# Kernel optimization log

Hardware: AMD Instinct MI355X
Metric: run time of the kernel (lower is better)

## Reference

```python
import jax, jax.numpy as jnp
import numpy as np

# (in_dim, hidden1, out_dim) for each torchvision MLP block
_DIMS = {"i": (3, 20, 100), "c": (10, 8, 1), "s": (17, 34, 17), "m": (100, 20, 100),
         "n": (100, 20, 100), "t": (200, 20, 100), "k": (300, 100, 100), "p": (100, 30, 3)}

def setup_inputs():
    key = jax.random.key(0)
    keys = iter(jax.random.split(key, 64))
    inp = {"x": jax.random.normal(next(keys), (14, 17, 10, 3), jnp.float32)}
    for p, (din, h1, h2) in _DIMS.items():
        inp[p + "W1"] = jax.random.normal(next(keys), (din, h1), jnp.float32) * 0.1
        inp[p + "b1"] = jnp.zeros((h1,), jnp.float32)
        inp[p + "g"] = jnp.ones((h1,), jnp.float32)
        inp[p + "B"] = jnp.zeros((h1,), jnp.float32)
        inp[p + "W2"] = jax.random.normal(next(keys), (h1, h2), jnp.float32) * 0.1
        inp[p + "b2"] = jnp.zeros((h2,), jnp.float32)
    return inp

def _ln(h, g, B):
    mu = jnp.mean(h, -1, keepdims=True)
    var = jnp.mean((h - mu) ** 2, -1, keepdims=True)
    return (h - mu) / jnp.sqrt(var + 1e-5) * g + B

def _mlp(x, W1, b1, g, B, W2, b2):
    # torchvision.ops.MLP([h1, h2]): Linear -> LayerNorm -> ReLU -> (dropout=id in eval) -> Linear
    h = jax.nn.relu(_ln(x @ W1 + b1, g, B))
    return h @ W2 + b2

def reference(x, iW1, ib1, ig, iB, iW2, ib2, cW1, cb1, cg, cB, cW2, cb2,
              sW1, sb1, sg, sB, sW2, sb2, mW1, mb1, mg, mB, mW2, mb2,
              nW1, nb1, ng, nB, nW2, nb2, tW1, tb1, tg, tB, tW2, tb2,
              kW1, kb1, kg, kB, kW2, kb2, pW1, pb1, pg, pB, pW2, pb2):
    h = _mlp(x, iW1, ib1, ig, iB, iW2, ib2)              # [14,17,10,100]
    h = jnp.swapaxes(h, -1, -2)                          # [14,17,100,10]
    h = _mlp(h, cW1, cb1, cg, cB, cW2, cb2)[..., 0]      # [14,17,100]
    h = jnp.swapaxes(h, -1, -2)                          # [14,100,17]
    h = _mlp(h, sW1, sb1, sg, sB, sW2, sb2)              # [14,100,17]
    h = jnp.swapaxes(h, -1, -2)                          # [14,17,100]
    # vectorized over the 10 center frames i = 2..11 (replaces the Python loop)
    mf = _mlp(h[1:11] - h[0:10], mW1, mb1, mg, mB, mW2, mb2)                      # [10,17,100]
    pf = _mlp(h[1:11], nW1, nb1, ng, nB, nW2, nb2)
    pf = _mlp(jnp.concatenate([pf, mf], -1), tW1, tb1, tg, tB, tW2, tb2)          # [10,17,100]
    mb_ = _mlp(h[4:14] - h[3:13], mW1, mb1, mg, mB, mW2, mb2)
    nf = _mlp(h[3:13], nW1, nb1, ng, nB, nW2, nb2)
    nf = _mlp(jnp.concatenate([nf, mb_], -1), tW1, tb1, tg, tB, tW2, tb2)         # [10,17,100]
    comb = _mlp(jnp.concatenate([pf, h[2:12], nf], -1), kW1, kb1, kg, kB, kW2, kb2)  # [10,17,100]
    # original writes out[0..9] of a zeros(12,17,100) buffer; rows 10,11 stay zero
    out = jnp.concatenate([comb, jnp.zeros((2, 17, 100), comb.dtype)], 0)         # [12,17,100]
    return _mlp(out, pW1, pb1, pg, pB, pW2, pb2)         # [12,17,3]
```

## Files before the change

### kernel.cpp

```cpp
#include <hip/hip_runtime.h>

#define T 512
#define NS1 70
#define ZBLK 240
#define FLAG_BYTE 98304
#define MAGIC 0x51A6E1D0C0FFEEULL

__device__ __forceinline__ float wave_sum_all(float v){
    #pragma unroll
    for (int off = 1; off < 64; off <<= 1) v += __shfl_xor(v, off, 64);
    return v;
}

__device__ __forceinline__ void cpa(const float* __restrict__ src, float* dst, int n, int t){
    int g4 = n >> 2;
    for (int g = t; g < g4; g += T) {
        __builtin_amdgcn_global_load_lds(
            (const __attribute__((address_space(1))) void*)(src + g*4),
            (__attribute__((address_space(3))) void*)(dst + g*4), 16, 0, 0);
    }
    for (int i = (g4<<2) + t; i < n; i += T) dst[i] = src[i];
}

struct S1 {
    alignas(16) float u[170][20];
    alignas(16) float h2s[17][20];
    alignas(16) float spre[20][34];
    alignas(16) float iW2[2000];
    alignas(16) float ib2[100];
    alignas(16) float cW1[80];
    alignas(16) float cb1[8];
    alignas(16) float cg[8];
    alignas(16) float cB[8];
    alignas(16) float cW2[8];
    alignas(16) float cb2s[4];
    alignas(16) float sW1[578];
    alignas(16) float sb1[36];
    alignas(16) float sg[36];
    alignas(16) float sB[36];
    alignas(16) float sW2[578];
    alignas(16) float sb2[20];
};
struct S2 {
    alignas(16) float inrow[4][100];
    alignas(16) float hid4[4][20];
    alignas(16) float v4[4][100];
    alignas(16) float hidT[2][20];
    alignas(16) float kin[300];
    alignas(16) float kpart[5][100];
    alignas(16) float khid[100];
    alignas(16) float comb[100];
    alignas(16) float ppart[4][32];
    alignas(16) float mW1[2000]; alignas(16) float mb1[20]; alignas(16) float mg[20];
    alignas(16) float mB[20];    alignas(16) float mW2[2000]; alignas(16) float mb2[100];
    alignas(16) float nW1[2000]; alignas(16) float nb1[20]; alignas(16) float ng[20];
    alignas(16) float nB[20];    alignas(16) float nW2[2000]; alignas(16) float nb2[100];
    alignas(16) float tW1[4000]; alignas(16) float tb1[20]; alignas(16) float tg[20];
    alignas(16) float tB[20];    alignas(16) float tW2[2000]; alignas(16) float tb2[100];
    alignas(16) float kb1[100];  alignas(16) float kg[100];  alignas(16) float kB[100];
    alignas(16) float kW2[10000]; alignas(16) float kb2[100];
    alignas(16) float pW1[3000]; alignas(16) float pb1[32]; alignas(16) float pg[32];
    alignas(16) float pB[32];    alignas(16) float pW2[92]; alignas(16) float pb2[4];
};
union SMem { S1 s1; S2 s2; };

__global__ __launch_bounds__(T) void k_fused(
    const float* __restrict__ x,
    const float* __restrict__ iW1, const float* __restrict__ ib1,
    const float* __restrict__ ig,  const float* __restrict__ iB,
    const float* __restrict__ iW2, const float* __restrict__ ib2,
    const float* __restrict__ cW1, const float* __restrict__ cb1,
    const float* __restrict__ cg,  const float* __restrict__ cB,
    const float* __restrict__ cW2, const float* __restrict__ cb2,
    const float* __restrict__ sW1, const float* __restrict__ sb1,
    const float* __restrict__ sg,  const float* __restrict__ sB,
    const float* __restrict__ sW2, const float* __restrict__ sb2,
    const float* __restrict__ mW1, const float* __restrict__ mb1,
    const float* __restrict__ mg,  const float* __restrict__ mB,
    const float* __restrict__ mW2, const float* __restrict__ mb2,
    const float* __restrict__ nW1, const float* __restrict__ nb1,
    const float* __restrict__ ng,  const float* __restrict__ nB,
    const float* __restrict__ nW2, const float* __restrict__ nb2,
    const float* __restrict__ tW1, const float* __restrict__ tb1,
    const float* __restrict__ tg,  const float* __restrict__ tB,
    const float* __restrict__ tW2, const float* __restrict__ tb2,
    const float* __restrict__ kW1, const float* __restrict__ kb1,
    const float* __restrict__ kg,  const float* __restrict__ kB,
    const float* __restrict__ kW2, const float* __restrict__ kb2,
    const float* __restrict__ pW1, const float* __restrict__ pb1,
    const float* __restrict__ pg,  const float* __restrict__ pB,
    const float* __restrict__ pW2, const float* __restrict__ pb2,
    float* __restrict__ h_ws, unsigned long long* __restrict__ flagS,
    float* __restrict__ out)
{
    const int bid = blockIdx.x;
    const int t = threadIdx.x;
    const int lane = t & 63, wv = t >> 6;
    __shared__ SMem sm;

    if (bid < NS1) {
        S1& s = sm.s1;
        cpa(iW2, s.iW2, 2000, t); cpa(ib2, s.ib2, 100, t);
        cpa(cW1, s.cW1, 80, t);   cpa(cb1, s.cb1, 8, t);  cpa(cg, s.cg, 8, t);
        cpa(cB, s.cB, 8, t);      cpa(cW2, s.cW2, 8, t);  cpa(cb2, s.cb2s, 1, t);
        cpa(sW1, s.sW1, 578, t);  cpa(sb1, s.sb1, 34, t); cpa(sg, s.sg, 34, t);
        cpa(sB, s.sB, 34, t);     cpa(sW2, s.sW2, 578, t); cpa(sb2, s.sb2, 17, t);

        const int a = bid / 5, d0 = (bid % 5) * 20;

        if (t < 170) {
            const float* xr = x + (a*170 + t)*3;
            float x0 = xr[0], x1 = xr[1], x2 = xr[2];
            float pre[20];
            float mu = 0.f;
            #pragma unroll
            for (int j = 0; j < 20; ++j) {
                float v = ib1[j] + x0*iW1[j] + x1*iW1[20+j] + x2*iW1[40+j];
                pre[j] = v; mu += v;
            }
            mu *= 0.05f;
            float var = 0.f;
            #pragma unroll
            for (int j = 0; j < 20; ++j) { float d = pre[j]-mu; var = fmaf(d,d,var); }
            float inv = rsqrtf(var*0.05f + 1e-5f);
            #pragma unroll
            for (int j = 0; j < 20; ++j) {
                float v = (pre[j]-mu)*inv*ig[j] + iB[j];
                s.u[t][j] = v > 0.f ? v : 0.f;
            }
        }
        __syncthreads();

        if (t < 340) {
            int b = t / 20, dd = t % 20, d = d0 + dd;
            float w[8];
            #pragma unroll
            for (int j = 0; j < 8; ++j) w[j] = s.cb1[j];
            float bias = s.ib2[d];
            #pragma unroll 2
            for (int c = 0; c < 10; ++c) {
                const float4* ur = (const float4*)s.u[b*10 + c];
                float4 u0=ur[0], u1=ur[1], u2=ur[2], u3=ur[3], u4=ur[4];
                float acc = bias;
                acc=fmaf(u0.x,s.iW2[0*100+d],acc);  acc=fmaf(u0.y,s.iW2[1*100+d],acc);
                acc=fmaf(u0.z,s.iW2[2*100+d],acc);  acc=fmaf(u0.w,s.iW2[3*100+d],acc);
                acc=fmaf(u1.x,s.iW2[4*100+d],acc);  acc=fmaf(u1.y,s.iW2[5*100+d],acc);
                acc=fmaf(u1.z,s.iW2[6*100+d],acc);  acc=fmaf(u1.w,s.iW2[7*100+d],acc);
                acc=fmaf(u2.x,s.iW2[8*100+d],acc);  acc=fmaf(u2.y,s.iW2[9*100+d],acc);
                acc=fmaf(u2.z,s.iW2[10*100+d],acc); acc=fmaf(u2.w,s.iW2[11*100+d],acc);
                acc=fmaf(u3.x,s.iW2[12*100+d],acc); acc=fmaf(u3.y,s.iW2[13*100+d],acc);
                acc=fmaf(u3.z,s.iW2[14*100+d],acc); acc=fmaf(u3.w,s.iW2[15*100+d],acc);
                acc=fmaf(u4.x,s.iW2[16*100+d],acc); acc=fmaf(u4.y,s.iW2[17*100+d],acc);
                acc=fmaf(u4.z,s.iW2[18*100+d],acc); acc=fmaf(u4.w,s.iW2[19*100+d],acc);
                #pragma unroll
                for (int j = 0; j < 8; ++j) w[j] = fmaf(acc, s.cW1[c*8+j], w[j]);
            }
            float mu = 0.f;
            #pragma unroll
            for (int j = 0; j < 8; ++j) mu += w[j];
            mu *= 0.125f;
            float var = 0.f;
            #pragma unroll
            for (int j = 0; j < 8; ++j) { float d2 = w[j]-mu; var = fmaf(d2,d2,var); }
            float inv = rsqrtf(var*0.125f + 1e-5f);
            float acc = s.cb2s[0];
            #pragma unroll
            for (int j = 0; j < 8; ++j) {
                float v = (w[j]-mu)*inv*s.cg[j] + s.cB[j];
                v = v > 0.f ? v : 0.f;
                acc = fmaf(v, s.cW2[j], acc);
            }
            s.h2s[b][dd] = acc;
        }
        __syncthreads();

        for (int o = t; o < 680; o += T) {
            int dd = o / 34, j = o % 34;
            float acc = s.sb1[j];
            #pragma unroll
            for (int b = 0; b < 17; ++b) acc = fmaf(s.h2s[b][dd], s.sW1[b*34+j], acc);
            s.spre[dd][j] = acc;
        }
        __syncthreads();

        for (int dd = wv; dd < 20; dd += 8) {
            float v = 0.f;
            if (lane < 34) v = s.spre[dd][lane];
            float mu = wave_sum_all(v) * (1.f/34.f);
            float d2 = (lane < 34) ? v - mu : 0.f;
            float inv = rsqrtf(wave_sum_all(d2*d2)*(1.f/34.f) + 1e-5f);
            if (lane < 34) {
                float r = d2*inv*s.sg[lane] + s.sB[lane];
                s.spre[dd][lane] = r > 0.f ? r : 0.f;
            }
            if (lane < 17) {
                float acc2 = s.sb2[lane];
                #pragma unroll
                for (int j = 0; j < 34; ++j)
                    acc2 = fmaf(s.spre[dd][j], s.sW2[j*17+lane], acc2);
                h_ws[a*1700 + lane*100 + d0 + dd] = acc2;
            }
        }
        __syncthreads();
        if (t == 0) {
            __builtin_amdgcn_fence(__ATOMIC_RELEASE, "agent");
            __hip_atomic_store(&flagS[bid*16], (unsigned long long)MAGIC,
                               __ATOMIC_RELAXED, __HIP_MEMORY_SCOPE_AGENT);
        }
        return;
    }

    S2& s = sm.s2;
    cpa(mW1, s.mW1, 2000, t); cpa(mb1, s.mb1, 20, t); cpa(mg, s.mg, 20, t);
    cpa(mB, s.mB, 20, t);     cpa(mW2, s.mW2, 2000, t); cpa(mb2, s.mb2, 100, t);
    cpa(nW1, s.nW1, 2000, t); cpa(nb1, s.nb1, 20, t); cpa(ng, s.ng, 20, t);
    cpa(nB, s.nB, 20, t);     cpa(nW2, s.nW2, 2000, t); cpa(nb2, s.nb2, 100, t);
    cpa(tW1, s.tW1, 4000, t); cpa(tb1, s.tb1, 20, t); cpa(tg, s.tg, 20, t);
    cpa(tB, s.tB, 20, t);     cpa(tW2, s.tW2, 2000, t); cpa(tb2, s.tb2, 100, t);
    cpa(kb1, s.kb1, 100, t);  cpa(kg, s.kg, 100, t);  cpa(kB, s.kB, 100, t);
    cpa(kW2, s.kW2, 10000, t); cpa(kb2, s.kb2, 100, t);
    cpa(pW1, s.pW1, 3000, t); cpa(pb1, s.pb1, 30, t); cpa(pg, s.pg, 30, t);
    cpa(pB, s.pB, 30, t);     cpa(pW2, s.pW2, 90, t); cpa(pb2, s.pb2, 3, t);

    const int task = bid - NS1;
    const int kq = t / 100, ko = t % 100;
    float wk[60];
    if (bid != ZBLK) {
        if (t < 500) {
            #pragma unroll
            for (int e = 0; e < 60; ++e) wk[e] = kW1[(kq*60+e)*100 + ko];
        }
        if (t < 64) {
            for (;;) {
                unsigned long long v1 = __hip_atomic_load(&flagS[t*16], __ATOMIC_RELAXED, __HIP_MEMORY_SCOPE_AGENT);
                unsigned long long v2 = (t < 6)
                    ? __hip_atomic_load(&flagS[(64+t)*16], __ATOMIC_RELAXED, __HIP_MEMORY_SCOPE_AGENT)
                    : (unsigned long long)MAGIC;
                if (__all(v1 == (unsigned long long)MAGIC && v2 == (unsigned long long)MAGIC)) break;
                __builtin_amdgcn_s_sleep(2);
            }
        }
    }
    __syncthreads();
    __builtin_amdgcn_fence(__ATOMIC_ACQUIRE, "agent");

    if (bid != ZBLK) {
        const int f = task / 17, b = task % 17;

        if (t < 100) {
            const float* hb = h_ws + b*100 + t;
            float h0  = hb[(f  )*1700];
            float h1v = hb[(f+1)*1700];
            float h2v = hb[(f+2)*1700];
            float h3v = hb[(f+3)*1700];
            float h4v = hb[(f+4)*1700];
            s.inrow[0][t] = h1v - h0;
            s.inrow[1][t] = h1v;
            s.inrow[2][t] = h4v - h3v;
            s.inrow[3][t] = h3v;
            s.kin[100+t]  = h2v;
        }
        __syncthreads();

        if (wv < 4) {
            bool is_m = !(wv & 1);
            const float* W1 = is_m ? s.mW1 : s.nW1;
            const float* b1 = is_m ? s.mb1 : s.nb1;
            const float* g  = is_m ? s.mg  : s.ng;
            const float* Bv = is_m ? s.mB  : s.nB;
            const float* W2 = is_m ? s.mW2 : s.nW2;
            const float* b2 = is_m ? s.mb2 : s.nb2;
            const float* in = s.inrow[wv];
            float v = 0.f;
            if (lane < 20) {
                float a0=0,a1=0,a2=0,a3=0;
                for (int e = 0; e < 100; e += 4) {
                    a0 = fmaf(in[e+0], W1[(e+0)*20+lane], a0);
                    a1 = fmaf(in[e+1], W1[(e+1)*20+lane], a1);
                    a2 = fmaf(in[e+2], W1[(e+2)*20+lane], a2);
                    a3 = fmaf(in[e+3], W1[(e+3)*20+lane], a3);
                }
                v = b1[lane] + ((a0+a1)+(a2+a3));
            }
            float mu = wave_sum_all((lane < 20) ? v : 0.f) * 0.05f;
            float dd = (lane < 20) ? v - mu : 0.f;
            float inv = rsqrtf(wave_sum_all(dd*dd)*0.05f + 1e-5f);
            if (lane < 20) {
                float r = dd*inv*g[lane] + Bv[lane];
                s.hid4[wv][lane] = r > 0.f ? r : 0.f;
            }
            {
                float acc0 = b2[lane];
                float acc1 = (lane < 36) ? b2[64+lane] : 0.f;
                #pragma unroll
                for (int j = 0; j < 20; ++j) {
                    float hj = s.hid4[wv][j];
                    acc0 = fmaf(hj, W2[j*100+lane], acc0);
                    if (lane < 36) acc1 = fmaf(hj, W2[j*100+64+lane], acc1);
                }
                s.v4[wv][lane] = acc0;
                if (lane < 36) s.v4[wv][64+lane] = acc1;
            }
        }
        __syncthreads();

        if (wv < 2) {
            const float* inA = wv ? s.v4[3] : s.v4[1];
            const float* inB = wv ? s.v4[2] : s.v4[0];
            float v = 0.f;
            if (lane < 20) {
                float a0=0,a1=0,a2=0,a3=0;
                for (int e = 0; e < 100; e += 4) {
                    a0 = fmaf(inA[e+0], s.tW1[(e+0)*20+lane], a0);
                    a1 = fmaf(inA[e+1], s.tW1[(e+1)*20+lane], a1);
                    a2 = fmaf(inA[e+2], s.tW1[(e+2)*20+lane], a2);
                    a3 = fmaf(inA[e+3], s.tW1[(e+3)*20+lane], a3);
                }
                for (int e = 0; e < 100; e += 4) {
                    a0 = fmaf(inB[e+0], s.tW1[(100+e+0)*20+lane], a0);
                    a1 = fmaf(inB[e+1], s.tW1[(100+e+1)*20+lane], a1);
                    a2 = fmaf(inB[e+2], s.tW1[(100+e+2)*20+lane], a2);
                    a3 = fmaf(inB[e+3], s.tW1[(100+e+3)*20+lane], a3);
                }
                v = s.tb1[lane] + ((a0+a1)+(a2+a3));
            }
            float mu = wave_sum_all((lane < 20) ? v : 0.f) * 0.05f;
            float dd = (lane < 20) ? v - mu : 0.f;
            float inv = rsqrtf(wave_sum_all(dd*dd)*0.05f + 1e-5f);
            if (lane < 20) {
                float r = dd*inv*s.tg[lane] + s.tB[lane];
                s.hidT[wv][lane] = r > 0.f ? r : 0.f;
            }
            {
                float acc0 = s.tb2[lane];
                float acc1 = (lane < 36) ? s.tb2[64+lane] : 0.f;
                #pragma unroll
                for (int j = 0; j < 20; ++j) {
                    float hj = s.hidT[wv][j];
                    acc0 = fmaf(hj, s.tW2[j*100+lane], acc0);
                    if (lane < 36) acc1 = fmaf(hj, s.tW2[j*100+64+lane], acc1);
                }
                s.kin[wv*200 + lane] = acc0;
                if (lane < 36) s.kin[wv*200 + 64+lane] = acc1;
            }
        }
        __syncthreads();

        if (t < 500) {
            const float* base = s.kin + kq*60;
            float a0=0.f, a1=0.f, a2=0.f;
            #pragma unroll
            for (int e = 0; e < 60; e += 3) {
                a0 = fmaf(base[e],   wk[e],   a0);
                a1 = fmaf(base[e+1], wk[e+1], a1);
                a2 = fmaf(base[e+2], wk[e+2], a2);
            }
            s.kpart[kq][ko] = a0 + a1 + a2;
        }
        __syncthreads();

        if (t < 64) {
            int l = t;
            float kv1 = s.kb1[l];
            #pragma unroll
            for (int q = 0; q < 5; ++q) kv1 += s.kpart[q][l];
            bool h36 = (l < 36);
            float kv2 = 0.f;
            if (h36) {
                kv2 = s.kb1[64+l];
                #pragma unroll
                for (int q = 0; q < 5; ++q) kv2 += s.kpart[q][64+l];
            }
            float mu = wave_sum_all(kv1 + (h36 ? kv2 : 0.f)) * 0.01f;
            float d1 = kv1 - mu, d2 = h36 ? kv2 - mu : 0.f;
            float var = wave_sum_all(fmaf(d1,d1,d2*d2)) * 0.01f;
            float inv = rsqrtf(var + 1e-5f);
            float r1 = d1*inv*s.kg[l] + s.kB[l];
            s.khid[l] = r1 > 0.f ? r1 : 0.f;
            if (h36) {
                float r2 = d2*inv*s.kg[64+l] + s.kB[64+l];
                s.khid[64+l] = r2 > 0.f ? r2 : 0.f;
            }
        }
        __syncthreads();

        if (t < 100) {
            float a0=0.f,a1=0.f,a2=0.f,a3=0.f;
            for (int j = 0; j < 100; j += 4) {
                a0 = fmaf(s.khid[j+0], s.kW2[(j+0)*100+t], a0);
                a1 = fmaf(s.khid[j+1], s.kW2[(j+1)*100+t], a1);
                a2 = fmaf(s.khid[j+2], s.kW2[(j+2)*100+t], a2);
                a3 = fmaf(s.khid[j+3], s.kW2[(j+3)*100+t], a3);
            }
            s.comb[t] = s.kb2[t] + ((a0+a1)+(a2+a3));
        }
        __syncthreads();

        if (t < 120) {
            int o = t % 30, q = t / 30, e0 = q*25;
            float a0 = 0.f;
            #pragma unroll
            for (int e = 0; e < 25; ++e)
                a0 = fmaf(s.comb[e0+e], s.pW1[(e0+e)*30+o], a0);
            s.ppart[q][o] = a0;
        }
        __syncthreads();

        if (t < 64) {
            int l = t;
            float v = 0.f;
            if (l < 30)
                v = s.pb1[l] + s.ppart[0][l] + s.ppart[1][l] + s.ppart[2][l] + s.ppart[3][l];
            float mu = wave_sum_all(v) * (1.f/30.f);
            float dd2 = (l < 30) ? v - mu : 0.f;
            float inv = rsqrtf(wave_sum_all(dd2*dd2)*(1.f/30.f) + 1e-5f);
            float pa = 0.f;
            if (l < 30) {
                pa = dd2*inv*s.pg[l] + s.pB[l];
                pa = pa > 0.f ? pa : 0.f;
            }
            float o0 = wave_sum_all((l < 30) ? pa*s.pW2[l*3+0] : 0.f);
            float o1 = wave_sum_all((l < 30) ? pa*s.pW2[l*3+1] : 0.f);
            float o2 = wave_sum_all((l < 30) ? pa*s.pW2[l*3+2] : 0.f);
            if (l == 0) {
                int r = f*17 + b;
                out[r*3+0] = s.pb2[0] + o0;
                out[r*3+1] = s.pb2[1] + o1;
                out[r*3+2] = s.pb2[2] + o2;
            }
        }
    } else {
        if (t < 64) {
            int l = t;
            float v = (l < 30) ? s.pb1[l] : 0.f;
            float mu = wave_sum_all(v) * (1.f/30.f);
            float dd2 = (l < 30) ? v - mu : 0.f;
            float inv = rsqrtf(wave_sum_all(dd2*dd2)*(1.f/30.f) + 1e-5f);
            float pa = 0.f;
            if (l < 30) {
                pa = dd2*inv*s.pg[l] + s.pB[l];
                pa = pa > 0.f ? pa : 0.f;
            }
            float o0 = s.pb2[0] + wave_sum_all((l < 30) ? pa*s.pW2[l*3+0] : 0.f);
            float o1 = s.pb2[1] + wave_sum_all((l < 30) ? pa*s.pW2[l*3+1] : 0.f);
            float o2 = s.pb2[2] + wave_sum_all((l < 30) ? pa*s.pW2[l*3+2] : 0.f);
            if (l < 34) {
                int r = 170 + l;
                out[r*3+0] = o0; out[r*3+1] = o1; out[r*3+2] = o2;
            }
        }
    }
}

extern "C" void kernel_launch(void* const* d_in, const int* in_sizes, int n_in,
                              void* d_out, int out_size, void* d_ws, size_t ws_size,
                              hipStream_t stream) {
    const float* x = (const float*)d_in[0];
    float* h = (float*)d_ws;
    unsigned long long* flags = (unsigned long long*)((char*)d_ws + FLAG_BYTE);
    #define P(i) ((const float*)d_in[i])
    k_fused<<<241, T, 0, stream>>>(x,
        P(1), P(2), P(3), P(4), P(5), P(6),
        P(7), P(8), P(9), P(10), P(11), P(12),
        P(13), P(14), P(15), P(16), P(17), P(18),
        P(19), P(20), P(21), P(22), P(23), P(24),
        P(25), P(26), P(27), P(28), P(29), P(30),
        P(31), P(32), P(33), P(34), P(35), P(36),
        P(37), P(38), P(39), P(40), P(41), P(42),
        P(43), P(44), P(45), P(46), P(47), P(48),
        h, flags, (float*)d_out);
    #undef P
}
```

Before: 30.42 us.

## Map one output row per wavefront in stage two, shrinking grid

The second stage now gives each wavefront one (frame, batch) row instead of a whole 512-thread block, so it needs 22 blocks instead of 171. Per-wave activation buffers in LDS replace the block-wide __syncthreads between sub-MLPs, and two 20-wide LayerNorms are packed into the two 32-lane halves of a wave. The kW1 weights are read straight from global memory by every wave instead of being preloaded into registers. In exchange, each wave does far more serial work and there is less parallelism per row. The padded zero rows are now handled by one wave.

New measurement: 33.19 us. +9.1%, slower.

```diff
diff --git a/kernel.cpp b/kernel.cpp
--- a/kernel.cpp
+++ b/kernel.cpp
@@ -2,13 +2,18 @@
 
 #define T 512
 #define NS1 70
-#define ZBLK 240
+#define NS2B 22
 #define FLAG_BYTE 98304
 #define MAGIC 0x51A6E1D0C0FFEEULL
 
 __device__ __forceinline__ float wave_sum_all(float v){
     #pragma unroll
     for (int off = 1; off < 64; off <<= 1) v += __shfl_xor(v, off, 64);
+    return v;
+}
+__device__ __forceinline__ float grp_sum32(float v){
+    #pragma unroll
+    for (int off = 1; off < 32; off <<= 1) v += __shfl_xor(v, off, 32);
     return v;
 }
 
@@ -41,16 +46,15 @@
     alignas(16) float sW2[578];
     alignas(16) float sb2[20];
 };
+struct WAct {
+    float inrow[4][100];
+    float kin[300];
+    float hid[4][20];
+    float hidT[2][20];
+    float v4[4][100];
+};
 struct S2 {
-    alignas(16) float inrow[4][100];
-    alignas(16) float hid4[4][20];
-    alignas(16) float v4[4][100];
-    alignas(16) float hidT[2][20];
-    alignas(16) float kin[300];
-    alignas(16) float kpart[5][100];
-    alignas(16) float khid[100];
-    alignas(16) float comb[100];
-    alignas(16) float ppart[4][32];
+    WAct w[8];
     alignas(16) float mW1[2000]; alignas(16) float mb1[20]; alignas(16) float mg[20];
     alignas(16) float mB[20];    alignas(16) float mW2[2000]; alignas(16) float mb2[100];
     alignas(16) float nW1[2000]; alignas(16) float nb1[20]; alignas(16) float ng[20];
@@ -222,232 +226,222 @@
     cpa(pW1, s.pW1, 3000, t); cpa(pb1, s.pb1, 30, t); cpa(pg, s.pg, 30, t);
     cpa(pB, s.pB, 30, t);     cpa(pW2, s.pW2, 90, t); cpa(pb2, s.pb2, 3, t);
 
-    const int task = bid - NS1;
-    const int kq = t / 100, ko = t % 100;
-    float wk[60];
-    if (bid != ZBLK) {
-        if (t < 500) {
-            #pragma unroll
-            for (int e = 0; e < 60; ++e) wk[e] = kW1[(kq*60+e)*100 + ko];
-        }
-        if (t < 64) {
-            for (;;) {
-                unsigned long long v1 = __hip_atomic_load(&flagS[t*16], __ATOMIC_RELAXED, __HIP_MEMORY_SCOPE_AGENT);
-                unsigned long long v2 = (t < 6)
-                    ? __hip_atomic_load(&flagS[(64+t)*16], __ATOMIC_RELAXED, __HIP_MEMORY_SCOPE_AGENT)
-                    : (unsigned long long)MAGIC;
-                if (__all(v1 == (unsigned long long)MAGIC && v2 == (unsigned long long)MAGIC)) break;
-                __builtin_amdgcn_s_sleep(2);
-            }
+    if (t < 64) {
+        for (;;) {
+            unsigned long long v1 = __hip_atomic_load(&flagS[t*16], __ATOMIC_RELAXED, __HIP_MEMORY_SCOPE_AGENT);
+            unsigned long long v2 = (t < 6)
+                ? __hip_atomic_load(&flagS[(64+t)*16], __ATOMIC_RELAXED, __HIP_MEMORY_SCOPE_AGENT)
+                : (unsigned long long)MAGIC;
+            if (__all(v1 == (unsigned long long)MAGIC && v2 == (unsigned long long)MAGIC)) break;
+            __builtin_amdgcn_s_sleep(2);
         }
     }
     __syncthreads();
     __builtin_amdgcn_fence(__ATOMIC_ACQUIRE, "agent");
 
-    if (bid != ZBLK) {
-        const int f = task / 17, b = task % 17;
-
-        if (t < 100) {
-            const float* hb = h_ws + b*100 + t;
+    const int gw = (bid - NS1)*8 + wv;
+    if (gw < 170) {
+        const int f = gw / 17, b = gw % 17;
+        WAct& ww = s.w[wv];
+
+        for (int o = lane; o < 100; o += 64) {
+            const float* hb = h_ws + b*100 + o;
             float h0  = hb[(f  )*1700];
             float h1v = hb[(f+1)*1700];
             float h2v = hb[(f+2)*1700];
             float h3v = hb[(f+3)*1700];
             float h4v = hb[(f+4)*1700];
-            s.inrow[0][t] = h1v - h0;
-            s.inrow[1][t] = h1v;
-            s.inrow[2][t] = h4v - h3v;
-            s.inrow[3][t] = h3v;
-            s.kin[100+t]  = h2v;
-        }
-        __syncthreads();
-
-        if (wv < 4) {
-            bool is_m = !(wv & 1);
-            const float* W1 = is_m ? s.mW1 : s.nW1;
-            const float* b1 = is_m ? s.mb1 : s.nb1;
-            const float* g  = is_m ? s.mg  : s.ng;
-            const float* Bv = is_m ? s.mB  : s.nB;
-            const float* W2 = is_m ? s.mW2 : s.nW2;
-            const float* b2 = is_m ? s.mb2 : s.nb2;
-            const float* in = s.inrow[wv];
-            float v = 0.f;
-            if (lane < 20) {
-                float a0=0,a1=0,a2=0,a3=0;
-                for (int e = 0; e < 100; e += 4) {
-                    a0 = fmaf(in[e+0], W1[(e+0)*20+lane], a0);
-                    a1 = fmaf(in[e+1], W1[(e+1)*20+lane], a1);
-                    a2 = fmaf(in[e+2], W1[(e+2)*20+lane], a2);
-                    a3 = fmaf(in[e+3], W1[(e+3)*20+lane], a3);
+            ww.inrow[0][o] = h1v - h0;
+            ww.inrow[1][o] = h1v;
+            ww.inrow[2][o] = h4v - h3v;
+            ww.inrow[3][o] = h3v;
+            ww.kin[100+o]  = h2v;
+        }
+
+        const int g = lane >> 5, lj = lane & 31;
+        {
+            const int rA = g*2, rB = rA + 1;
+            float preA = 0.f, preB = 0.f;
+            if (lj < 20) {
+                const float* inA_ = ww.inrow[rA];
+                const float* inB_ = ww.inrow[rB];
+                float a0=0,a1=0,b0=0,b1=0;
+                for (int e = 0; e < 100; e += 2) {
+                    a0 = fmaf(inA_[e],   s.mW1[(e  )*20+lj], a0);
+                    a1 = fmaf(inA_[e+1], s.mW1[(e+1)*20+lj], a1);
+                    b0 = fmaf(inB_[e],   s.nW1[(e  )*20+lj], b0);
+                    b1 = fmaf(inB_[e+1], s.nW1[(e+1)*20+lj], b1);
                 }
-                v = b1[lane] + ((a0+a1)+(a2+a3));
-            }
-            float mu = wave_sum_all((lane < 20) ? v : 0.f) * 0.05f;
-            float dd = (lane < 20) ? v - mu : 0.f;
-            float inv = rsqrtf(wave_sum_all(dd*dd)*0.05f + 1e-5f);
-            if (lane < 20) {
-                float r = dd*inv*g[lane] + Bv[lane];
-                s.hid4[wv][lane] = r > 0.f ? r : 0.f;
-            }
-            {
-                float acc0 = b2[lane];
-                float acc1 = (lane < 36) ? b2[64+lane] : 0.f;
+                preA = s.mb1[lj] + a0 + a1;
+                preB = s.nb1[lj] + b0 + b1;
+            }
+            float muA = grp_sum32((lj<20)?preA:0.f) * 0.05f;
+            float dA = (lj<20)? preA-muA : 0.f;
+            float invA = rsqrtf(grp_sum32(dA*dA)*0.05f + 1e-5f);
+            float muB = grp_sum32((lj<20)?preB:0.f) * 0.05f;
+            float dB = (lj<20)? preB-muB : 0.f;
+            float invB = rsqrtf(grp_sum32(dB*dB)*0.05f + 1e-5f);
+            if (lj < 20) {
+                float hA = dA*invA*s.mg[lj] + s.mB[lj];
+                float hB = dB*invB*s.ng[lj] + s.nB[lj];
+                ww.hid[rA][lj] = hA > 0.f ? hA : 0.f;
+                ww.hid[rB][lj] = hB > 0.f ? hB : 0.f;
+            }
+        }
+        {
+            const int o1 = lane;
+            const int o2 = (lane < 36) ? 64+lane : 64;
+            #pragma unroll
+            for (int r = 0; r < 4; ++r) {
+                const bool im = !(r & 1);
+                const float* W2  = im ? s.mW2 : s.nW2;
+                const float* b2v = im ? s.mb2 : s.nb2;
+                float acc0 = b2v[o1], acc1 = b2v[o2];
                 #pragma unroll
                 for (int j = 0; j < 20; ++j) {
-                    float hj = s.hid4[wv][j];
-                    acc0 = fmaf(hj, W2[j*100+lane], acc0);
-                    if (lane < 36) acc1 = fmaf(hj, W2[j*100+64+lane], acc1);
+                    float hj = ww.hid[r][j];
+                    acc0 = fmaf(hj, W2[j*100+o1], acc0);
+                    acc1 = fmaf(hj, W2[j*100+o2], acc1);
                 }
-                s.v4[wv][lane] = acc0;
-                if (lane < 36) s.v4[wv][64+lane] = acc1;
-            }
-        }
-        __syncthreads();
-
-        if (wv < 2) {
-            const float* inA = wv ? s.v4[3] : s.v4[1];
-            const float* inB = wv ? s.v4[2] : s.v4[0];
-            float v = 0.f;
-            if (lane < 20) {
+                ww.v4[r][o1] = acc0;
+                if (lane < 36) ww.v4[r][o2] = acc1;
+            }
+        }
+
+        {
+            float preT = 0.f;
+            if (lj < 20) {
+                const float* inA_ = g ? ww.v4[3] : ww.v4[1];
+                const float* inB_ = g ? ww.v4[2] : ww.v4[0];
                 float a0=0,a1=0,a2=0,a3=0;
-                for (int e = 0; e < 100; e += 4) {
-                    a0 = fmaf(inA[e+0], s.tW1[(e+0)*20+lane], a0);
-                    a1 = fmaf(inA[e+1], s.tW1[(e+1)*20+lane], a1);
-                    a2 = fmaf(inA[e+2], s.tW1[(e+2)*20+lane], a2);
-                    a3 = fmaf(inA[e+3], s.tW1[(e+3)*20+lane], a3);
+                for (int e = 0; e < 100; e += 2) {
+                    a0 = fmaf(inA_[e],   s.tW1[(e    )*20+lj], a0);
+                    a1 = fmaf(inA_[e+1], s.tW1[(e+1  )*20+lj], a1);
+                    a2 = fmaf(inB_[e],   s.tW1[(100+e)*20+lj], a2);
+                    a3 = fmaf(inB_[e+1], s.tW1[(101+e)*20+lj], a3);
                 }
-                for (int e = 0; e < 100; e += 4) {
-                    a0 = fmaf(inB[e+0], s.tW1[(100+e+0)*20+lane], a0);
-                    a1 = fmaf(inB[e+1], s.tW1[(100+e+1)*20+lane], a1);
-                    a2 = fmaf(inB[e+2], s.tW1[(100+e+2)*20+lane], a2);
-                    a3 = fmaf(inB[e+3], s.tW1[(100+e+3)*20+lane], a3);
-                }
-                v = s.tb1[lane] + ((a0+a1)+(a2+a3));
-            }
-            float mu = wave_sum_all((lane < 20) ? v : 0.f) * 0.05f;
-            float dd = (lane < 20) ? v - mu : 0.f;
-            float inv = rsqrtf(wave_sum_all(dd*dd)*0.05f + 1e-5f);
-            if (lane < 20) {
-                float r = dd*inv*s.tg[lane] + s.tB[lane];
-                s.hidT[wv][lane] = r > 0.f ? r : 0.f;
-            }
-            {
-                float acc0 = s.tb2[lane];
-                float acc1 = (lane < 36) ? s.tb2[64+lane] : 0.f;
+                preT = s.tb1[lj] + ((a0+a1)+(a2+a3));
+            }
+            float muT = grp_sum32((lj<20)?preT:0.f) * 0.05f;
+            float dT = (lj<20)? preT-muT : 0.f;
+            float invT = rsqrtf(grp_sum32(dT*dT)*0.05f + 1e-5f);
+            if (lj < 20) {
+                float hT = dT*invT*s.tg[lj] + s.tB[lj];
+                ww.hidT[g][lj] = hT > 0.f ? hT : 0.f;
+            }
+        }
+        {
+            const int o1 = lane;
+            const int o2 = (lane < 36) ? 64+lane : 64;
+            #pragma unroll
+            for (int r = 0; r < 2; ++r) {
+                float acc0 = s.tb2[o1], acc1 = s.tb2[o2];
                 #pragma unroll
                 for (int j = 0; j < 20; ++j) {
-                    float hj = s.hidT[wv][j];
-                    acc0 = fmaf(hj, s.tW2[j*100+lane], acc0);
-                    if (lane < 36) acc1 = fmaf(hj, s.tW2[j*100+64+lane], acc1);
+                    float hj = ww.hidT[r][j];
+                    acc0 = fmaf(hj, s.tW2[j*100+o1], acc0);
+                    acc1 = fmaf(hj, s.tW2[j*100+o2], acc1);
                 }
-                s.kin[wv*200 + lane] = acc0;
-                if (lane < 36) s.kin[wv*200 + 64+lane] = acc1;
-            }
-        }
-        __syncthreads();
-
-        if (t < 500) {
-            const float* base = s.kin + kq*60;
-            float a0=0.f, a1=0.f, a2=0.f;
-            #pragma unroll
-            for (int e = 0; e < 60; e += 3) {
-                a0 = fmaf(base[e],   wk[e],   a0);
-                a1 = fmaf(base[e+1], wk[e+1], a1);
-                a2 = fmaf(base[e+2], wk[e+2], a2);
-            }
-            s.kpart[kq][ko] = a0 + a1 + a2;
-        }
-        __syncthreads();
-
-        if (t < 64) {
-            int l = t;
-            float kv1 = s.kb1[l];
-            #pragma unroll
-            for (int q = 0; q < 5; ++q) kv1 += s.kpart[q][l];
-            bool h36 = (l < 36);
-            float kv2 = 0.f;
-            if (h36) {
-                kv2 = s.kb1[64+l];
-                #pragma unroll
-                for (int q = 0; q < 5; ++q) kv2 += s.kpart[q][64+l];
-            }
-            float mu = wave_sum_all(kv1 + (h36 ? kv2 : 0.f)) * 0.01f;
-            float d1 = kv1 - mu, d2 = h36 ? kv2 - mu : 0.f;
+                ww.kin[r*200+o1] = acc0;
+                if (lane < 36) ww.kin[r*200+o2] = acc1;
+            }
+        }
+
+        const int o1 = lane;
+        const int o2 = (lane < 36) ? 64+lane : 64;
+        float kv1, kv2;
+        {
+            float a0=0,a1=0,a2=0,a3=0, c0=0,c1=0,c2=0,c3=0;
+            for (int e = 0; e < 300; e += 4) {
+                float k0=ww.kin[e], k1=ww.kin[e+1], k2=ww.kin[e+2], k3=ww.kin[e+3];
+                a0 = fmaf(k0, kW1[(e  )*100+o1], a0);
+                a1 = fmaf(k1, kW1[(e+1)*100+o1], a1);
+                a2 = fmaf(k2, kW1[(e+2)*100+o1], a2);
+                a3 = fmaf(k3, kW1[(e+3)*100+o1], a3);
+                c0 = fmaf(k0, kW1[(e  )*100+o2], c0);
+                c1 = fmaf(k1, kW1[(e+1)*100+o2], c1);
+                c2 = fmaf(k2, kW1[(e+2)*100+o2], c2);
+                c3 = fmaf(k3, kW1[(e+3)*100+o2], c3);
+            }
+            kv1 = s.kb1[o1] + ((a0+a1)+(a2+a3));
+            kv2 = (lane < 36) ? s.kb1[o2] + ((c0+c1)+(c2+c3)) : 0.f;
+        }
+        float* khidw = ww.v4[0];
+        float* combw = ww.v4[1];
+        {
+            float mu = wave_sum_all(kv1 + kv2) * 0.01f;
+            float d1 = kv1 - mu, d2 = (lane < 36) ? kv2 - mu : 0.f;
             float var = wave_sum_all(fmaf(d1,d1,d2*d2)) * 0.01f;
             float inv = rsqrtf(var + 1e-5f);
-            float r1 = d1*inv*s.kg[l] + s.kB[l];
-            s.khid[l] = r1 > 0.f ? r1 : 0.f;
-            if (h36) {
-                float r2 = d2*inv*s.kg[64+l] + s.kB[64+l];
-                s.khid[64+l] = r2 > 0.f ? r2 : 0.f;
-            }
-        }
-        __syncthreads();
-
-        if (t < 100) {
-            float a0=0.f,a1=0.f,a2=0.f,a3=0.f;
+            float r1 = d1*inv*s.kg[o1] + s.kB[o1];
+            khidw[o1] = r1 > 0.f ? r1 : 0.f;
+            if (lane < 36) {
+                float r2 = d2*inv*s.kg[o2] + s.kB[o2];
+                khidw[o2] = r2 > 0.f ? r2 : 0.f;
+            }
+        }
+        {
+            float b0=0,b1=0,b2a=0,b3=0, e0=0,e1=0,e2=0,e3=0;
             for (int j = 0; j < 100; j += 4) {
-                a0 = fmaf(s.khid[j+0], s.kW2[(j+0)*100+t], a0);
-                a1 = fmaf(s.khid[j+1], s.kW2[(j+1)*100+t], a1);
-                a2 = fmaf(s.khid[j+2], s.kW2[(j+2)*100+t], a2);
-                a3 = fmaf(s.khid[j+3], s.kW2[(j+3)*100+t], a3);
-            }
-            s.comb[t] = s.kb2[t] + ((a0+a1)+(a2+a3));
-        }
-        __syncthreads();
-
-        if (t < 120) {
-            int o = t % 30, q = t / 30, e0 = q*25;
-            float a0 = 0.f;
-            #pragma unroll
-            for (int e = 0; e < 25; ++e)
-                a0 = fmaf(s.comb[e0+e], s.pW1[(e0+e)*30+o], a0);
-            s.ppart[q][o] = a0;
-        }
-        __syncthreads();
-
-        if (t < 64) {
-            int l = t;
-            float v = 0.f;
-            if (l < 30)
-                v = s.pb1[l] + s.ppart[0][l] + s.ppart[1][l] + s.ppart[2][l] + s.ppart[3][l];
-            float mu = wave_sum_all(v) * (1.f/30.f);
-            float dd2 = (l < 30) ? v - mu : 0.f;
-            float inv = rsqrtf(wave_sum_all(dd2*dd2)*(1.f/30.f) + 1e-5f);
+                float h0=khidw[j], h1=khidw[j+1], h2=khidw[j+2], h3=khidw[j+3];
+                b0  = fmaf(h0, s.kW2[(j  )*100+o1], b0);
+                b1  = fmaf(h1, s.kW2[(j+1)*100+o1], b1);
+                b2a = fmaf(h2, s.kW2[(j+2)*100+o1], b2a);
+                b3  = fmaf(h3, s.kW2[(j+3)*100+o1], b3);
+                e0  = fmaf(h0, s.kW2[(j  )*100+o2], e0);
+                e1  = fmaf(h1, s.kW2[(j+1)*100+o2], e1);
+                e2  = fmaf(h2, s.kW2[(j+2)*100+o2], e2);
+                e3  = fmaf(h3, s.kW2[(j+3)*100+o2], e3);
+            }
+            combw[o1] = s.kb2[o1] + ((b0+b1)+(b2a+b3));
+            if (lane < 36) combw[o2] = s.kb2[o2] + ((e0+e1)+(e2+e3));
+        }
+        {
+            float pv = 0.f;
+            if (lane < 30) {
+                float q0=0,q1=0,q2=0,q3=0;
+                for (int e = 0; e < 100; e += 4) {
+                    q0 = fmaf(combw[e],   s.pW1[(e  )*30+lane], q0);
+                    q1 = fmaf(combw[e+1], s.pW1[(e+1)*30+lane], q1);
+                    q2 = fmaf(combw[e+2], s.pW1[(e+2)*30+lane], q2);
+                    q3 = fmaf(combw[e+3], s.pW1[(e+3)*30+lane], q3);
+                }
+                pv = s.pb1[lane] + ((q0+q1)+(q2+q3));
+            }
+            float pmu = wave_sum_all((lane<30)?pv:0.f) * (1.f/30.f);
+            float pd = (lane<30)? pv - pmu : 0.f;
+            float pinv = rsqrtf(wave_sum_all(pd*pd)*(1.f/30.f) + 1e-5f);
             float pa = 0.f;
-            if (l < 30) {
-                pa = dd2*inv*s.pg[l] + s.pB[l];
+            if (lane < 30) {
+                pa = pd*pinv*s.pg[lane] + s.pB[lane];
                 pa = pa > 0.f ? pa : 0.f;
             }
-            float o0 = wave_sum_all((l < 30) ? pa*s.pW2[l*3+0] : 0.f);
-            float o1 = wave_sum_all((l < 30) ? pa*s.pW2[l*3+1] : 0.f);
-            float o2 = wave_sum_all((l < 30) ? pa*s.pW2[l*3+2] : 0.f);
-            if (l == 0) {
+            float s0 = wave_sum_all((lane<30)? pa*s.pW2[lane*3+0] : 0.f);
+            float s1v = wave_sum_all((lane<30)? pa*s.pW2[lane*3+1] : 0.f);
+            float s2v = wave_sum_all((lane<30)? pa*s.pW2[lane*3+2] : 0.f);
+            if (lane == 0) {
                 int r = f*17 + b;
-                out[r*3+0] = s.pb2[0] + o0;
-                out[r*3+1] = s.pb2[1] + o1;
-                out[r*3+2] = s.pb2[2] + o2;
-            }
-        }
-    } else {
-        if (t < 64) {
-            int l = t;
-            float v = (l < 30) ? s.pb1[l] : 0.f;
-            float mu = wave_sum_all(v) * (1.f/30.f);
-            float dd2 = (l < 30) ? v - mu : 0.f;
-            float inv = rsqrtf(wave_sum_all(dd2*dd2)*(1.f/30.f) + 1e-5f);
-            float pa = 0.f;
-            if (l < 30) {
-                pa = dd2*inv*s.pg[l] + s.pB[l];
-                pa = pa > 0.f ? pa : 0.f;
-            }
-            float o0 = s.pb2[0] + wave_sum_all((l < 30) ? pa*s.pW2[l*3+0] : 0.f);
-            float o1 = s.pb2[1] + wave_sum_all((l < 30) ? pa*s.pW2[l*3+1] : 0.f);
-            float o2 = s.pb2[2] + wave_sum_all((l < 30) ? pa*s.pW2[l*3+2] : 0.f);
-            if (l < 34) {
-                int r = 170 + l;
-                out[r*3+0] = o0; out[r*3+1] = o1; out[r*3+2] = o2;
-            }
+                out[r*3+0] = s.pb2[0] + s0;
+                out[r*3+1] = s.pb2[1] + s1v;
+                out[r*3+2] = s.pb2[2] + s2v;
+            }
+        }
+    } else if (gw == 170) {
+        float pv = (lane < 30) ? s.pb1[lane] : 0.f;
+        float pmu = wave_sum_all(pv) * (1.f/30.f);
+        float pd = (lane<30)? pv - pmu : 0.f;
+        float pinv = rsqrtf(wave_sum_all(pd*pd)*(1.f/30.f) + 1e-5f);
+        float pa = 0.f;
+        if (lane < 30) {
+            pa = pd*pinv*s.pg[lane] + s.pB[lane];
+            pa = pa > 0.f ? pa : 0.f;
+        }
+        float s0 = s.pb2[0] + wave_sum_all((lane<30)? pa*s.pW2[lane*3+0] : 0.f);
+        float s1v = s.pb2[1] + wave_sum_all((lane<30)? pa*s.pW2[lane*3+1] : 0.f);
+        float s2v = s.pb2[2] + wave_sum_all((lane<30)? pa*s.pW2[lane*3+2] : 0.f);
+        if (lane < 34) {
+            int r = 170 + lane;
+            out[r*3+0] = s0; out[r*3+1] = s1v; out[r*3+2] = s2v;
         }
     }
 }
@@ -459,7 +453,7 @@
     float* h = (float*)d_ws;
     unsigned long long* flags = (unsigned long long*)((char*)d_ws + FLAG_BYTE);
     #define P(i) ((const float*)d_in[i])
-    k_fused<<<241, T, 0, stream>>>(x,
+    k_fused<<<NS1 + NS2B, T, 0, stream>>>(x,
         P(1), P(2), P(3), P(4), P(5), P(6),
         P(7), P(8), P(9), P(10), P(11), P(12),
         P(13), P(14), P(15), P(16), P(17), P(18),
```
